# Optimization experiments

Measured on AMD Instinct MI355X. Metric: run time of the kernel, lower is better.

Reference implementation:

```python
import jax, jax.numpy as jnp
import numpy as np

B, L, E, H = 2, 2048, 1024, 16
D = E // H  # head_dim = 64


def setup_inputs() -> dict:
    key = jax.random.key(0)
    ks = jax.random.split(key, 9)
    s = 1.0 / np.sqrt(E)
    return {
        "query": jax.random.normal(ks[0], (B, L, E), jnp.float32),
        "key": jax.random.normal(ks[1], (B, L, E), jnp.float32),
        "value": jax.random.normal(ks[2], (B, L, E), jnp.float32),
        # torch Linear weights are [out_features, in_features]
        "Wq": jax.random.uniform(ks[3], (E, E), jnp.float32, -s, s),
        "bq": jnp.zeros((E,), jnp.float32),
        "Wk": jax.random.uniform(ks[4], (E, E), jnp.float32, -s, s),  # k_proj, no bias (add_bias_kv=False)
        "Wv": jax.random.uniform(ks[5], (E, E), jnp.float32, -s, s),  # v_proj, no bias
        "Wo": jax.random.uniform(ks[6], (E, E), jnp.float32, -s, s),
        "bo": jnp.zeros((E,), jnp.float32),
    }


def reference(query, key, value, Wq, bq, Wk, Wv, Wo, bo):
    # Projections (torch Linear: y = x @ W.T + b)
    q = query @ Wq.T + bq          # [B, L, E]
    k = key @ Wk.T                 # [B, L, E]
    v = value @ Wv.T               # [B, L, E]
    # Split heads
    q = q.reshape(B, L, H, D)
    k = k.reshape(B, L, H, D)
    v = v.reshape(B, L, H, D)
    # Scaled dot-product attention; the source's chunked online-softmax
    # computes exactly softmax(q k^T / sqrt(D)) v.
    q = q / jnp.sqrt(jnp.asarray(D, q.dtype))
    scores = jnp.einsum("bqhd,bkhd->bhqk", q, k)      # [B, H, L, L]
    probs = jax.nn.softmax(scores, axis=-1)
    out = jnp.einsum("bhqk,bkhd->bqhd", probs, v)     # [B, L, H, D]
    out = out.reshape(B, L, E)
    return out @ Wo.T + bo
```

## Files before the change

### kernel.cpp

```cpp
#include <hip/hip_runtime.h>

typedef __bf16 bf16;
typedef __bf16 bf16x8 __attribute__((ext_vector_type(8)));
typedef __bf16 bf16x4 __attribute__((ext_vector_type(4)));
typedef float  f32x4  __attribute__((ext_vector_type(4)));

#define MFMA_BF16(a, b, c) __builtin_amdgcn_mfma_f32_16x16x32_bf16((a), (b), (c), 0, 0, 0)


__device__ __forceinline__ void async_load16(const bf16* g, const bf16* l) {
    auto gp = (const __attribute__((address_space(1))) unsigned int*)(unsigned long long)(const void*)g;
    auto lp = (__attribute__((address_space(3))) unsigned int*)(unsigned int)(unsigned long long)(const void*)l;
    __builtin_amdgcn_global_load_lds(gp, lp, 16, 0, 0);
}

__global__ void cvt_bf16_kernel(
    const float* __restrict__ s0, const float* __restrict__ s1, const float* __restrict__ s2,
    const float* __restrict__ s3, const float* __restrict__ s4, const float* __restrict__ s5,
    const float* __restrict__ s6,
    bf16* __restrict__ d0, bf16* __restrict__ d1, bf16* __restrict__ d2,
    bf16* __restrict__ d3, bf16* __restrict__ d4, bf16* __restrict__ d5,
    bf16* __restrict__ d6)
{
    unsigned e = (blockIdx.x * 256 + threadIdx.x) * 4;
    const float* src; bf16* dst; unsigned off;
    if (e < 12582912u) {
        unsigned which = e >> 22;
        src = which == 0 ? s0 : (which == 1 ? s1 : s2);
        dst = which == 0 ? d0 : (which == 1 ? d1 : d2);
        off = e & 4194303u;
    } else {
        unsigned ew = e - 12582912u;
        unsigned which = ew >> 20;
        src = which == 0 ? s3 : (which == 1 ? s4 : (which == 2 ? s5 : s6));
        dst = which == 0 ? d3 : (which == 1 ? d4 : (which == 2 ? d5 : d6));
        off = ew & 1048575u;
    }
    float4 f = *(const float4*)(src + off);
    bf16x4 o;
    o.x = (bf16)f.x; o.y = (bf16)f.y; o.z = (bf16)f.z; o.w = (bf16)f.w;
    *(bf16x4*)(dst + off) = o;
}

template<int BN>
__global__ __launch_bounds__(256, (BN == 128) ? 2 : 4) void gemm4_kernel(
    const bf16* __restrict__ Xq, const bf16* __restrict__ Xk, const bf16* __restrict__ Xv,
    const bf16* __restrict__ Ao,
    const bf16* __restrict__ Wq, const bf16* __restrict__ Wk, const bf16* __restrict__ Wv,
    const bf16* __restrict__ Wo,
    const float* __restrict__ bq, const float* __restrict__ bo,
    bf16* __restrict__ Qs, bf16* __restrict__ Ksw, bf16* __restrict__ Vsw,
    float* __restrict__ out, int zbase)
{
    const int z = zbase + blockIdx.z;
    const bf16 *Amat, *Bmat;
    if (z == 0)      { Amat = Wq; Bmat = Xq; }
    else if (z == 1) { Amat = Wk; Bmat = Xk; }
    else if (z == 2) { Amat = Xv; Bmat = Wv; }
    else             { Amat = Wo; Bmat = Ao; }

    const int flat = blockIdx.x + 8 * blockIdx.y;
    const int c    = flat & 7;
    const int j    = flat >> 3;
    const int ft   = j & 7;
    const int tt   = c * (gridDim.y >> 3) + (j >> 3);

    const int m0 = (z == 2 ? tt : ft) * 128;
    const int n0 = (z == 2 ? ft : tt) * BN;

    __shared__ __align__(16) bf16 lA[2][128 * 32];
    __shared__ __align__(16) bf16 lB[2][BN * 32];

    const int tid  = threadIdx.x;
    const int w    = tid >> 6;
    const int lane = tid & 63;
    const int lm   = lane & 15;
    const int g    = lane >> 4;
    const int wm   = (w & 1) * 64;
    const int wn   = (w >> 1) * (BN / 2);
    constexpr int NT = BN / 32;
    constexpr int T  = (128 + BN) / 64;

    f32x4 acc[4][NT] = {};

    for (int kb2 = 0; kb2 < 16; kb2++) {
        __syncthreads();
#pragma unroll
        for (int st = 0; st < 2; st++) {
            int kb = kb2 * 2 + st;
#pragma unroll
            for (int t = 0; t < T; t++) {
                int s   = (t * 4 + w) * 64 + lane;
                int row = s >> 2;
                int gs  = s & 3;
                int gg  = gs ^ ((row >> 1) & 3);
                if (row < 128)
                    async_load16(Amat + (size_t)(m0 + row) * 1024 + kb * 32 + gg * 8,
                                 lA[st] + s * 8);
                else
                    async_load16(Bmat + (size_t)(n0 + row - 128) * 1024 + kb * 32 + gg * 8,
                                 lB[st] + (s - 512) * 8);
            }
        }
        __syncthreads();

#pragma unroll
        for (int st = 0; st < 2; st++) {
            bf16x8 af[4], bfr[NT];
#pragma unroll
            for (int mt = 0; mt < 4; mt++) {
                int row = wm + mt * 16 + lm;
                af[mt] = *(const bf16x8*)(lA[st] + row * 32 + ((g ^ ((row >> 1) & 3)) << 3));
            }
#pragma unroll
            for (int nt = 0; nt < NT; nt++) {
                int row = wn + nt * 16 + lm;
                bfr[nt] = *(const bf16x8*)(lB[st] + row * 32 + ((g ^ ((row >> 1) & 3)) << 3));
            }
#pragma unroll
            for (int mt = 0; mt < 4; mt++)
#pragma unroll
                for (int nt = 0; nt < NT; nt++)
                    acc[mt][nt] = MFMA_BF16(af[mt], bfr[nt], acc[mt][nt]);
        }
    }

    if (z == 3) {
#pragma unroll
        for (int mt = 0; mt < 4; mt++) {
            int mb = m0 + wm + mt * 16 + g * 4;
            f32x4 bov = *(const f32x4*)(bo + mb);
#pragma unroll
            for (int nt = 0; nt < NT; nt++) {
                int n = n0 + wn + nt * 16 + lm;
                f32x4 val;
#pragma unroll
                for (int r = 0; r < 4; r++) val[r] = acc[mt][nt][r] + bov[r];
                *(f32x4*)(out + (size_t)n * 1024 + mb) = val;
            }
        }
    } else if (z == 2) {
#pragma unroll
        for (int mt = 0; mt < 4; mt++) {
            int mb   = m0 + wm + mt * 16 + g * 4;
            int b    = mb >> 11;
            int lpos = mb & 2047;
            int kb2  = lpos >> 6, kc = (lpos >> 5) & 1, gv = (lpos >> 3) & 3, j0 = lpos & 7;
#pragma unroll
            for (int nt = 0; nt < NT; nt++) {
                int n = n0 + wn + nt * 16 + lm;
                int h = n >> 6, mt2 = (n >> 4) & 3, lmv = n & 15;
                bf16x4 ov;
#pragma unroll
                for (int r = 0; r < 4; r++) ov[r] = (bf16)acc[mt][nt][r];
                *(bf16x4*)(Vsw + (size_t)(b * 16 + h) * 131072 +
                           (size_t)((kb2 * 8 + mt2 * 2 + kc) * 64 + gv * 16 + lmv) * 8 + j0) = ov;
            }
        }
    } else if (z == 1) {
#pragma unroll
        for (int mt = 0; mt < 4; mt++) {
            int mb = m0 + wm + mt * 16 + g * 4;
            int h  = mb >> 6;
            int f  = (mb >> 5) & 1, gk = (mb >> 3) & 3, j0 = mb & 7;
#pragma unroll
            for (int nt = 0; nt < NT; nt++) {
                int n    = n0 + wn + nt * 16 + lm;
                int b    = n >> 11;
                int lpos = n & 2047;
                int kb2  = lpos >> 6;
                int rem  = lpos & 63;
                int cc   = ((rem >> 4) & 2) | ((rem >> 2) & 1);
                int lmk  = ((rem >> 1) & 12) | (rem & 3);
                bf16x4 ov;
#pragma unroll
                for (int r = 0; r < 4; r++) ov[r] = (bf16)acc[mt][nt][r];
                *(bf16x4*)(Ksw + (size_t)(b * 16 + h) * 131072 +
                           (size_t)((kb2 * 8 + cc * 2 + f) * 64 + gk * 16 + lmk) * 8 + j0) = ov;
            }
        }
    } else {
        const float qscale = 0.18033688011112042f;
#pragma unroll
        for (int mt = 0; mt < 4; mt++) {
            int mb  = m0 + wm + mt * 16 + g * 4;
            int h   = mb >> 6;
            int dd0 = mb & 63;
            f32x4 bqv = *(const f32x4*)(bq + mb);
#pragma unroll
            for (int nt = 0; nt < NT; nt++) {
                int n    = n0 + wn + nt * 16 + lm;
                int b    = n >> 11;
                int lpos = n & 2047;
                bf16x4 ov;
#pragma unroll
                for (int r = 0; r < 4; r++)
                    ov[r] = (bf16)((acc[mt][nt][r] + bqv[r]) * qscale);
                *(bf16x4*)(Qs + (size_t)((b * 16 + h) * 2048 + lpos) * 64 + dd0) = ov;
            }
        }
    }
}

__global__ __launch_bounds__(256, 2) void attn_kernel(
    const bf16* __restrict__ Qs, const bf16* __restrict__ Ksw,
    const bf16* __restrict__ Vsw, bf16* __restrict__ attn)
{
    const int tid  = threadIdx.x;
    const int w    = tid >> 6;
    const int lane = tid & 63;
    const int lm   = lane & 15;
    const int g    = lane >> 4;
    const int i    = blockIdx.x;
    const int bh   = ((i & 7) << 2) | ((i >> 3) & 3);
    const int q0   = (i >> 5) * 128 + w * 32;

    const bf16* Qh = Qs  + (size_t)bh * 131072;
    const bf16* Kh = Ksw + (size_t)bh * 131072;
    const bf16* Vh = Vsw + (size_t)bh * 131072;

    __shared__ __align__(16) bf16 kbuf[3][4096];
    __shared__ __align__(16) bf16 vbuf[3][4096];
    __shared__ __align__(16) bf16 ost[4][32 * 72];

    bf16x8 qf[2][2];
#pragma unroll
    for (int qi = 0; qi < 2; qi++)
#pragma unroll
        for (int f = 0; f < 2; f++)
            qf[qi][f] = *(const bf16x8*)(Qh + (size_t)(q0 + qi * 16 + lm) * 64 + f * 32 + g * 8);

#define STAGE(sb, buf)                                                          \
    do {                                                                        \
        _Pragma("unroll")                                                       \
        for (int t = 0; t < 4; t++) {                                           \
            int slot = w * 4 + t;                                               \
            if (slot < 8)                                                       \
                async_load16(Kh + ((size_t)((sb) * 8 + slot) * 64 + lane) * 8,  \
                             kbuf[buf] + (slot * 64 + lane) * 8);               \
            else                                                                \
                async_load16(Vh + ((size_t)((sb) * 8 + slot - 8) * 64 + lane) * 8, \
                             vbuf[buf] + ((slot - 8) * 64 + lane) * 8);         \
        }                                                                       \
    } while (0)

    STAGE(0, 0);
    STAGE(1, 1);

    const f32x4 fzero = {0.0f, 0.0f, 0.0f, 0.0f};
    f32x4 o[2][4] = {};
    float lsum[2] = {0.0f, 0.0f};

    int cur = 0;
    for (int kb = 0; kb < 32; kb++) {
        if (kb < 31)
            asm volatile("s_waitcnt vmcnt(4)" ::: "memory");
        else
            asm volatile("s_waitcnt vmcnt(0)" ::: "memory");
        __builtin_amdgcn_s_barrier();
        __builtin_amdgcn_sched_barrier(0);

        if (kb < 30) {
            int nb = cur + 2; if (nb >= 3) nb -= 3;
            STAGE(kb + 2, nb);
        }

        const bf16* kc_ = kbuf[cur];
        const bf16* vc_ = vbuf[cur];

        f32x4 s[2][4];
        __builtin_amdgcn_s_setprio(1);
#pragma unroll
        for (int c = 0; c < 4; c++) {
            bf16x8 kf0 = *(const bf16x8*)(kc_ + ((c * 2 + 0) * 64 + lane) * 8);
            bf16x8 kf1 = *(const bf16x8*)(kc_ + ((c * 2 + 1) * 64 + lane) * 8);
            s[0][c] = MFMA_BF16(kf0, qf[0][0], fzero);
            s[1][c] = MFMA_BF16(kf0, qf[1][0], fzero);
            s[0][c] = MFMA_BF16(kf1, qf[0][1], s[0][c]);
            s[1][c] = MFMA_BF16(kf1, qf[1][1], s[1][c]);
        }
        __builtin_amdgcn_s_setprio(0);

        bf16x8 pb[2][2];
#pragma unroll
        for (int qi = 0; qi < 2; qi++) {
            float part = 0.0f;
#pragma unroll
            for (int kc = 0; kc < 2; kc++)
#pragma unroll
                for (int r = 0; r < 4; r++) {
                    float p0 = __builtin_amdgcn_exp2f(s[qi][2 * kc][r]);
                    float p1 = __builtin_amdgcn_exp2f(s[qi][2 * kc + 1][r]);
                    pb[qi][kc][r]     = (bf16)p0;
                    pb[qi][kc][r + 4] = (bf16)p1;
                    part += p0 + p1;
                }
            lsum[qi] += part;
        }

        __builtin_amdgcn_s_setprio(1);
#pragma unroll
        for (int kc = 0; kc < 2; kc++)
#pragma unroll
            for (int mt = 0; mt < 4; mt++) {
                bf16x8 vf = *(const bf16x8*)(vc_ + ((mt * 2 + kc) * 64 + lane) * 8);
                o[0][mt] = MFMA_BF16(vf, pb[0][kc], o[0][mt]);
                o[1][mt] = MFMA_BF16(vf, pb[1][kc], o[1][mt]);
            }
        __builtin_amdgcn_s_setprio(0);

        cur += 1; if (cur >= 3) cur -= 3;
    }
#undef STAGE

#pragma unroll
    for (int qi = 0; qi < 2; qi++) {
        lsum[qi] += __shfl_xor(lsum[qi], 16);
        lsum[qi] += __shfl_xor(lsum[qi], 32);
    }

    const int b = bh >> 4, h = bh & 15;
#pragma unroll
    for (int qi = 0; qi < 2; qi++) {
        float inv = 1.0f / lsum[qi];
#pragma unroll
        for (int mt = 0; mt < 4; mt++) {
            bf16x4 ov;
#pragma unroll
            for (int r = 0; r < 4; r++) ov[r] = (bf16)(o[qi][mt][r] * inv);
            *(bf16x4*)(ost[w] + (qi * 16 + lm) * 72 + mt * 16 + g * 4) = ov;
        }
    }
#pragma unroll
    for (int it = 0; it < 4; it++) {
        int cc = it * 64 + lane;
        int q  = cc >> 3, ch = cc & 7;
        bf16x8 t = *(const bf16x8*)(ost[w] + q * 72 + ch * 8);
        *(bf16x8*)(attn + (size_t)(b * 2048 + q0 + q) * 1024 + h * 64 + ch * 8) = t;
    }
}

extern "C" void kernel_launch(void* const* d_in, const int* in_sizes, int n_in,
                              void* d_out, int out_size, void* d_ws, size_t ws_size,
                              hipStream_t stream) {
    const float* query = (const float*)d_in[0];
    const float* key   = (const float*)d_in[1];
    const float* value = (const float*)d_in[2];
    const float* Wq    = (const float*)d_in[3];
    const float* bq    = (const float*)d_in[4];
    const float* Wk    = (const float*)d_in[5];
    const float* Wv    = (const float*)d_in[6];
    const float* Wo    = (const float*)d_in[7];
    const float* bo    = (const float*)d_in[8];

    char* ws = (char*)d_ws;
    bf16* Xq  = (bf16*)(ws);
    bf16* Xk  = (bf16*)(ws + ((size_t)8  << 20));
    bf16* Xv  = (bf16*)(ws + ((size_t)16 << 20));
    bf16* Wqb = (bf16*)(ws + ((size_t)24 << 20));
    bf16* Wkb = (bf16*)(ws + ((size_t)26 << 20));
    bf16* Wvb = (bf16*)(ws + ((size_t)28 << 20));
    bf16* Wob = (bf16*)(ws + ((size_t)30 << 20));
    bf16* Qs  = (bf16*)(ws + ((size_t)32 << 20));
    bf16* Ksw = (bf16*)(ws + ((size_t)40 << 20));
    bf16* Vsw = (bf16*)(ws + ((size_t)48 << 20));
    bf16* attn = Xq;

    cvt_bf16_kernel<<<dim3(16384, 1, 1), 256, 0, stream>>>(
        query, key, value, Wq, Wk, Wv, Wo, Xq, Xk, Xv, Wqb, Wkb, Wvb, Wob);

    gemm4_kernel<128><<<dim3(8, 32, 3), 256, 0, stream>>>(
        Xq, Xk, Xv, attn, Wqb, Wkb, Wvb, Wob, bq, bo, Qs, Ksw, Vsw, (float*)d_out, 0);

    attn_kernel<<<dim3(512, 1, 1), 256, 0, stream>>>(Qs, Ksw, Vsw, attn);

    gemm4_kernel<64><<<dim3(8, 64, 1), 256, 0, stream>>>(
        Xq, Xk, Xv, attn, Wqb, Wkb, Wvb, Wob, bq, bo, Qs, Ksw, Vsw, (float*)d_out, 3);
}
```

Before: 205.1 us.

## Split attention block across eight waves with 16 query rows each

```diff
diff --git a/kernel.cpp b/kernel.cpp
--- a/kernel.cpp
+++ b/kernel.cpp
@@ -202,7 +202,7 @@
     }
 }
 
-__global__ __launch_bounds__(256, 2) void attn_kernel(
+__global__ __launch_bounds__(512, 4) void attn_kernel(
     const bf16* __restrict__ Qs, const bf16* __restrict__ Ksw,
     const bf16* __restrict__ Vsw, bf16* __restrict__ attn)
 {
@@ -213,48 +213,44 @@
     const int g    = lane >> 4;
     const int i    = blockIdx.x;
     const int bh   = ((i & 7) << 2) | ((i >> 3) & 3);
-    const int q0   = (i >> 5) * 128 + w * 32;
+    const int q0   = (i >> 5) * 128 + w * 16;
 
     const bf16* Qh = Qs  + (size_t)bh * 131072;
     const bf16* Kh = Ksw + (size_t)bh * 131072;
     const bf16* Vh = Vsw + (size_t)bh * 131072;
 
-    __shared__ __align__(16) bf16 kbuf[3][4096];
-    __shared__ __align__(16) bf16 vbuf[3][4096];
-    __shared__ __align__(16) bf16 ost[4][32 * 72];
-
-    bf16x8 qf[2][2];
-#pragma unroll
-    for (int qi = 0; qi < 2; qi++)
-#pragma unroll
-        for (int f = 0; f < 2; f++)
-            qf[qi][f] = *(const bf16x8*)(Qh + (size_t)(q0 + qi * 16 + lm) * 64 + f * 32 + g * 8);
-
-#define STAGE(sb, buf)                                                          \
-    do {                                                                        \
-        _Pragma("unroll")                                                       \
-        for (int t = 0; t < 4; t++) {                                           \
-            int slot = w * 4 + t;                                               \
-            if (slot < 8)                                                       \
-                async_load16(Kh + ((size_t)((sb) * 8 + slot) * 64 + lane) * 8,  \
-                             kbuf[buf] + (slot * 64 + lane) * 8);               \
-            else                                                                \
+    __shared__ __align__(16) bf16 smem[24576];
+
+    bf16x8 qf[2];
+#pragma unroll
+    for (int f = 0; f < 2; f++)
+        qf[f] = *(const bf16x8*)(Qh + (size_t)(q0 + lm) * 64 + f * 32 + g * 8);
+
+#define STAGE(sb, buf)                                                             \
+    do {                                                                           \
+        _Pragma("unroll")                                                          \
+        for (int t = 0; t < 2; t++) {                                              \
+            int slot = w * 2 + t;                                                  \
+            if (slot < 8)                                                          \
+                async_load16(Kh + ((size_t)((sb) * 8 + slot) * 64 + lane) * 8,     \
+                             smem + (buf) * 4096 + (slot * 64 + lane) * 8);        \
+            else                                                                   \
                 async_load16(Vh + ((size_t)((sb) * 8 + slot - 8) * 64 + lane) * 8, \
-                             vbuf[buf] + ((slot - 8) * 64 + lane) * 8);         \
-        }                                                                       \
+                             smem + 12288 + (buf) * 4096 + ((slot - 8) * 64 + lane) * 8); \
+        }                                                                          \
     } while (0)
 
     STAGE(0, 0);
     STAGE(1, 1);
 
     const f32x4 fzero = {0.0f, 0.0f, 0.0f, 0.0f};
-    f32x4 o[2][4] = {};
-    float lsum[2] = {0.0f, 0.0f};
+    f32x4 o[4] = {};
+    float lsum = 0.0f;
 
     int cur = 0;
     for (int kb = 0; kb < 32; kb++) {
         if (kb < 31)
-            asm volatile("s_waitcnt vmcnt(4)" ::: "memory");
+            asm volatile("s_waitcnt vmcnt(2)" ::: "memory");
         else
             asm volatile("s_waitcnt vmcnt(0)" ::: "memory");
         __builtin_amdgcn_s_barrier();
@@ -265,38 +261,33 @@
             STAGE(kb + 2, nb);
         }
 
-        const bf16* kc_ = kbuf[cur];
-        const bf16* vc_ = vbuf[cur];
-
-        f32x4 s[2][4];
+        const bf16* kc_ = smem + cur * 4096;
+        const bf16* vc_ = smem + 12288 + cur * 4096;
+
+        f32x4 s[4];
         __builtin_amdgcn_s_setprio(1);
 #pragma unroll
         for (int c = 0; c < 4; c++) {
             bf16x8 kf0 = *(const bf16x8*)(kc_ + ((c * 2 + 0) * 64 + lane) * 8);
             bf16x8 kf1 = *(const bf16x8*)(kc_ + ((c * 2 + 1) * 64 + lane) * 8);
-            s[0][c] = MFMA_BF16(kf0, qf[0][0], fzero);
-            s[1][c] = MFMA_BF16(kf0, qf[1][0], fzero);
-            s[0][c] = MFMA_BF16(kf1, qf[0][1], s[0][c]);
-            s[1][c] = MFMA_BF16(kf1, qf[1][1], s[1][c]);
+            s[c] = MFMA_BF16(kf0, qf[0], fzero);
+            s[c] = MFMA_BF16(kf1, qf[1], s[c]);
         }
         __builtin_amdgcn_s_setprio(0);
 
-        bf16x8 pb[2][2];
-#pragma unroll
-        for (int qi = 0; qi < 2; qi++) {
-            float part = 0.0f;
-#pragma unroll
-            for (int kc = 0; kc < 2; kc++)
-#pragma unroll
-                for (int r = 0; r < 4; r++) {
-                    float p0 = __builtin_amdgcn_exp2f(s[qi][2 * kc][r]);
-                    float p1 = __builtin_amdgcn_exp2f(s[qi][2 * kc + 1][r]);
-                    pb[qi][kc][r]     = (bf16)p0;
-                    pb[qi][kc][r + 4] = (bf16)p1;
-                    part += p0 + p1;
-                }
-            lsum[qi] += part;
-        }
+        bf16x8 pb[2];
+        float part = 0.0f;
+#pragma unroll
+        for (int kc = 0; kc < 2; kc++)
+#pragma unroll
+            for (int r = 0; r < 4; r++) {
+                float p0 = __builtin_amdgcn_exp2f(s[2 * kc][r]);
+                float p1 = __builtin_amdgcn_exp2f(s[2 * kc + 1][r]);
+                pb[kc][r]     = (bf16)p0;
+                pb[kc][r + 4] = (bf16)p1;
+                part += p0 + p1;
+            }
+        lsum += part;
 
         __builtin_amdgcn_s_setprio(1);
 #pragma unroll
@@ -304,8 +295,7 @@
 #pragma unroll
             for (int mt = 0; mt < 4; mt++) {
                 bf16x8 vf = *(const bf16x8*)(vc_ + ((mt * 2 + kc) * 64 + lane) * 8);
-                o[0][mt] = MFMA_BF16(vf, pb[0][kc], o[0][mt]);
-                o[1][mt] = MFMA_BF16(vf, pb[1][kc], o[1][mt]);
+                o[mt] = MFMA_BF16(vf, pb[kc], o[mt]);
             }
         __builtin_amdgcn_s_setprio(0);
 
@@ -313,29 +303,26 @@
     }
 #undef STAGE
 
-#pragma unroll
-    for (int qi = 0; qi < 2; qi++) {
-        lsum[qi] += __shfl_xor(lsum[qi], 16);
-        lsum[qi] += __shfl_xor(lsum[qi], 32);
-    }
+    lsum += __shfl_xor(lsum, 16);
+    lsum += __shfl_xor(lsum, 32);
+
+    __syncthreads();
+    bf16* ostw = smem + w * 1152;
 
     const int b = bh >> 4, h = bh & 15;
-#pragma unroll
-    for (int qi = 0; qi < 2; qi++) {
-        float inv = 1.0f / lsum[qi];
-#pragma unroll
-        for (int mt = 0; mt < 4; mt++) {
-            bf16x4 ov;
-#pragma unroll
-            for (int r = 0; r < 4; r++) ov[r] = (bf16)(o[qi][mt][r] * inv);
-            *(bf16x4*)(ost[w] + (qi * 16 + lm) * 72 + mt * 16 + g * 4) = ov;
-        }
-    }
-#pragma unroll
-    for (int it = 0; it < 4; it++) {
+    float inv = 1.0f / lsum;
+#pragma unroll
+    for (int mt = 0; mt < 4; mt++) {
+        bf16x4 ov;
+#pragma unroll
+        for (int r = 0; r < 4; r++) ov[r] = (bf16)(o[mt][r] * inv);
+        *(bf16x4*)(ostw + lm * 72 + mt * 16 + g * 4) = ov;
+    }
+#pragma unroll
+    for (int it = 0; it < 2; it++) {
         int cc = it * 64 + lane;
         int q  = cc >> 3, ch = cc & 7;
-        bf16x8 t = *(const bf16x8*)(ost[w] + q * 72 + ch * 8);
+        bf16x8 t = *(const bf16x8*)(ostw + q * 72 + ch * 8);
         *(bf16x8*)(attn + (size_t)(b * 2048 + q0 + q) * 1024 + h * 64 + ch * 8) = t;
     }
 }
@@ -372,7 +359,7 @@
     gemm4_kernel<128><<<dim3(8, 32, 3), 256, 0, stream>>>(
         Xq, Xk, Xv, attn, Wqb, Wkb, Wvb, Wob, bq, bo, Qs, Ksw, Vsw, (float*)d_out, 0);
 
-    attn_kernel<<<dim3(512, 1, 1), 256, 0, stream>>>(Qs, Ksw, Vsw, attn);
+    attn_kernel<<<dim3(512, 1, 1), 512, 0, stream>>>(Qs, Ksw, Vsw, attn);
 
     gemm4_kernel<64><<<dim3(8, 64, 1), 256, 0, stream>>>(
         Xq, Xk, Xv, attn, Wqb, Wkb, Wvb, Wob, bq, bo, Qs, Ksw, Vsw, (float*)d_out, 3);
```

Measured after the change: 209.4 us. 1.02x slower.
